# Kernel tuning notes

Hardware: AMD Instinct MI355X
Metric: run time of the kernel (lower is better)

The kernel has to match this reference:

```python
import jax, jax.numpy as jnp
import numpy as np

B, L, D, H = 2, 2048, 2048, 16
DH = D // H

def setup_inputs() -> dict:
    key = jax.random.key(0)
    ks = jax.random.split(key, 7)
    q = jax.random.normal(ks[0], (B, L, D), dtype=jnp.float32)
    k = jax.random.normal(ks[1], (B, L, D), dtype=jnp.float32)
    v = jax.random.normal(ks[2], (B, L, D), dtype=jnp.float32)
    # causal mask: True means masked (matches torch masked_fill semantics)
    attn_mask = jnp.triu(jnp.ones((L, L), dtype=bool), k=1)[None, None, :, :]
    scale = 0.02
    wq = jax.random.normal(ks[3], (D, D), dtype=jnp.float32) * scale
    wk = jax.random.normal(ks[4], (D, D), dtype=jnp.float32) * scale
    wv = jax.random.normal(ks[5], (D, D), dtype=jnp.float32) * scale
    wo = jax.random.normal(ks[6], (D, D), dtype=jnp.float32) * scale
    return {"q": q, "k": k, "v": v, "attn_mask": attn_mask,
            "wq": wq, "wk": wk, "wv": wv, "wo": wo}

def _split_heads(x):
    b, l, _ = x.shape
    return x.reshape(b, l, H, DH).transpose(0, 2, 1, 3)  # [B,H,L,DH]

def reference(q, k, v, attn_mask, wq, wk, wv, wo):
    # torch Linear: y = x @ W.T (bias=False)
    qh = _split_heads(q @ wq.T)
    kh = _split_heads(k @ wk.T)
    vh = _split_heads(v @ wv.T)
    scale = 1.0 / np.sqrt(DH).astype(np.float32)
    scores = jnp.einsum('bhqd,bhkd->bhqk', qh, kh) * scale
    neg = jnp.finfo(scores.dtype).min
    scores = jnp.where(attn_mask, neg, scores)
    attn = jax.nn.softmax(scores, axis=-1)
    ctx = jnp.einsum('bhqk,bhkd->bhqd', attn, vh)
    ctx = ctx.transpose(0, 2, 1, 3).reshape(q.shape[0], q.shape[1], D)
    return ctx @ wo.T
```

## Files before the change

### kernel.cpp

```cpp
#include <hip/hip_runtime.h>

#define B_  2
#define L_  2048
#define D_  2048
#define H_  16
#define DH_ 128
#define K_  2048

#define SCALEQ_ 0.12751734f

typedef __attribute__((ext_vector_type(8))) short bf16x8;
typedef __attribute__((ext_vector_type(4))) float f32x4;
typedef __attribute__((ext_vector_type(4))) float float4v;
typedef __attribute__((ext_vector_type(8))) unsigned short u16x8;
typedef __attribute__((ext_vector_type(4))) unsigned short u16x4;

__device__ __forceinline__ unsigned short f2bf(float f) {
  unsigned u = __builtin_bit_cast(unsigned, f);
  u += 0x7fffu + ((u >> 16) & 1u);
  return (unsigned short)(u >> 16);
}

__device__ __forceinline__ float exp2i(float x) {
  float r;
  asm("v_exp_f32 %0, %1" : "=v"(r) : "v"(x));
  return r;
}

typedef __attribute__((address_space(3))) unsigned int lds_uint;
typedef __attribute__((address_space(1))) const unsigned int glob_uint;
__device__ __forceinline__ void gld16(const void* g, void* l) {
  __builtin_amdgcn_global_load_lds((glob_uint*)g, (lds_uint*)l, 16, 0, 0);
}

#define BAR() do { asm volatile("" ::: "memory"); __builtin_amdgcn_s_barrier(); asm volatile("" ::: "memory"); } while (0)
#define VMCNT(n) asm volatile("s_waitcnt vmcnt(" #n ")" ::: "memory")

__global__ void cvt_all(const float* __restrict__ wq, const float* __restrict__ wk,
                        const float* __restrict__ wv, const float* __restrict__ wo,
                        const float* __restrict__ q, const float* __restrict__ k,
                        const float* __restrict__ v, unsigned short* __restrict__ ws,
                        int nacts) {
  const size_t DD = (size_t)D_ * D_;
  const size_t BLD = (size_t)B_ * L_ * D_;
  const int z = blockIdx.z;
  const float* src;
  unsigned short* dst;
  size_t nelem;
  if (z < 4) {
    src = (z == 0) ? wq : (z == 1) ? wk : (z == 2) ? wv : wo;
    dst = ws + (size_t)z * DD;
    nelem = DD;
  } else {
    if (z - 4 >= nacts) return;
    src = (z == 4) ? q : (z == 5) ? k : v;
    dst = ws + 4 * DD + (size_t)(z - 4) * BLD;
    nelem = BLD;
  }
  size_t i = ((size_t)blockIdx.x * 256 + threadIdx.x) * 8;
  if (i >= nelem) return;
  float4v x0 = *(const float4v*)(src + i);
  float4v x1 = *(const float4v*)(src + i + 4);
  u16x8 p;
  p[0]=f2bf(x0[0]); p[1]=f2bf(x0[1]); p[2]=f2bf(x0[2]); p[3]=f2bf(x0[3]);
  p[4]=f2bf(x1[0]); p[5]=f2bf(x1[1]); p[6]=f2bf(x1[2]); p[7]=f2bf(x1[3]);
  *(u16x8*)(dst + i) = p;
}

__global__ __launch_bounds__(512, 2) void gemm256(
    const unsigned short* __restrict__ a0, const unsigned short* __restrict__ a1,
    const unsigned short* __restrict__ w0, const unsigned short* __restrict__ w1,
    unsigned short* __restrict__ Kh, unsigned short* __restrict__ Vt) {
  __shared__ unsigned short smem[2 * 32768];

  const int lin = blockIdx.x + 16 * (blockIdx.y + 8 * blockIdx.z);
  const int s = (lin & 7) * 32 + (lin >> 3);
  const int mt = s & 15;
  const int r_ = s >> 4;
  const int ntile = r_ & 7;
  const int z = r_ >> 3;

  const unsigned short* A = z ? a1 : a0;
  const unsigned short* W = z ? w1 : w0;

  const int bm0 = mt * 256;
  const int bn0 = ntile * 256;

  const int tid = threadIdx.x;
  const int wid = tid >> 6, lane = tid & 63;
  const int wr = wid >> 2;
  const int wc = wid & 3;
  const int l15 = lane & 15, l4 = lane >> 4;

  const unsigned short* gsrc[8];
  int ldst[8];
#pragma unroll
  for (int i = 0; i < 4; ++i) {
    const int c = i * 512 + tid, r = c >> 3, s0 = c & 7;
    gsrc[i] = A + (size_t)(bm0 + r) * K_ + ((s0 ^ (r & 7)) << 3);
    ldst[i] = c * 8;
    gsrc[4 + i] = W + (size_t)(bn0 + r) * K_ + ((s0 ^ (r & 7)) << 3);
    ldst[4 + i] = 16384 + c * 8;
  }
#define STAGE(idx, p) do { gld16(gsrc[idx], &smem[(p) * 32768 + ldst[idx]]); gsrc[idx] += 64; } while (0)

  int offA[8][2], offB[4][2];
#pragma unroll
  for (int mf = 0; mf < 8; ++mf)
#pragma unroll
    for (int ks = 0; ks < 2; ++ks) {
      const int row = wr * 128 + mf * 16 + l15;
      const int ch = ks * 4 + l4;
      offA[mf][ks] = row * 64 + ((ch ^ (row & 7)) << 3);
    }
#pragma unroll
  for (int nf = 0; nf < 4; ++nf)
#pragma unroll
    for (int ks = 0; ks < 2; ++ks) {
      const int rowb = wc * 64 + nf * 16 + l15;
      const int ch = ks * 4 + l4;
      offB[nf][ks] = 16384 + rowb * 64 + ((ch ^ (rowb & 7)) << 3);
    }

  f32x4 acc[8][4];
#pragma unroll
  for (int m = 0; m < 8; ++m)
#pragma unroll
    for (int n = 0; n < 4; ++n) { f32x4 zz = {0.f, 0.f, 0.f, 0.f}; acc[m][n] = zz; }

  STAGE(0, 0); STAGE(1, 0); STAGE(2, 0); STAGE(3, 0);
  STAGE(4, 0); STAGE(5, 0); STAGE(6, 0); STAGE(7, 0);
  VMCNT(0);
  BAR();

  int p = 0;
  for (int t = 0; t < 32; ++t) {
    const int p2 = p ^ 1;
    if (t < 31) {
      STAGE(0, p2); STAGE(1, p2); STAGE(2, p2); STAGE(3, p2);
      STAGE(4, p2); STAGE(5, p2); STAGE(6, p2); STAGE(7, p2);
    }
    const unsigned short* bA = &smem[p * 32768];
    bf16x8 bfr[4][2];
#pragma unroll
    for (int nf = 0; nf < 4; ++nf)
#pragma unroll
      for (int ks = 0; ks < 2; ++ks)
        bfr[nf][ks] = *(const bf16x8*)&bA[offB[nf][ks]];
    __builtin_amdgcn_s_setprio(1);
#pragma unroll
    for (int mf = 0; mf < 8; ++mf) {
      bf16x8 a0f = *(const bf16x8*)&bA[offA[mf][0]];
      bf16x8 a1f = *(const bf16x8*)&bA[offA[mf][1]];
#pragma unroll
      for (int nf = 0; nf < 4; ++nf) {
        acc[mf][nf] = __builtin_amdgcn_mfma_f32_16x16x32_bf16(a0f, bfr[nf][0], acc[mf][nf], 0, 0, 0);
        acc[mf][nf] = __builtin_amdgcn_mfma_f32_16x16x32_bf16(a1f, bfr[nf][1], acc[mf][nf], 0, 0, 0);
      }
    }
    __builtin_amdgcn_s_setprio(0);
    VMCNT(0);
    BAR();
    p = p2;
  }
#undef STAGE

  if (z == 0) {
#pragma unroll
    for (int mf = 0; mf < 8; ++mf) {
      const int rr = bm0 + wr * 128 + mf * 16 + l4 * 4;
#pragma unroll
      for (int nf = 0; nf < 4; ++nf) {
        const int cc = bn0 + wc * 64 + nf * 16 + l15;
        const int h = cc >> 7, dh = cc & 127;
#pragma unroll
        for (int j = 0; j < 4; ++j) {
          const int r2 = rr + j;
          Kh[((size_t)((r2 >> 11) * H_ + h) * L_ + (r2 & 2047)) * DH_ + dh] = f2bf(acc[mf][nf][j]);
        }
      }
    }
  } else {
    unsigned short* T = smem;
    const int b = bm0 >> 11, lb = bm0 & 2047;
#pragma unroll 1
    for (int half = 0; half < 2; ++half) {
      if (half) __syncthreads();
      if (wr == half) {
#pragma unroll
        for (int mf = 0; mf < 8; ++mf) {
          const int rl = mf * 16 + l4 * 4;
#pragma unroll
          for (int nf = 0; nf < 4; ++nf) {
            const int cl = wc * 64 + nf * 16 + l15;
            u16x4 vv;
#pragma unroll
            for (int j = 0; j < 4; ++j) vv[j] = f2bf(acc[mf][nf][j]);
            *(u16x4*)&T[cl * 144 + rl] = vv;
          }
        }
      }
      __syncthreads();
#pragma unroll
      for (int it = 0; it < 8; ++it) {
        const int idx = it * 512 + tid;
        const int rT = idx >> 4, cT = idx & 15;
        u16x8 val = *(const u16x8*)&T[rT * 144 + cT * 8];
        const int n = bn0 + rT, h = n >> 7, dh = n & 127;
        *(u16x8*)&Vt[((size_t)(b * H_ + h) * DH_ + dh) * L_ + lb + half * 128 + cT * 8] = val;
      }
    }
  }
}

template <int OUT>
__global__ __launch_bounds__(512, 2) void gemm8p(
    const unsigned short* __restrict__ A, const unsigned short* __restrict__ W,
    void* __restrict__ outp) {
  __shared__ unsigned short smem[3 * 24576];

  const int lin = blockIdx.x + 32 * blockIdx.y;
  const int s = (lin & 7) * 32 + (lin >> 3);
  const int mt = s & 31;
  const int ntile = s >> 5;

  const int bm0 = mt * 128;
  const int bn0 = ntile * 256;

  const int tid = threadIdx.x;
  const int wid = tid >> 6, lane = tid & 63;
  const int wr = wid >> 2, wc = wid & 3;
  const int l15 = lane & 15, l4 = lane >> 4;

  const unsigned short* gsrc[6];
  int ldst[6];
  {
#pragma unroll
    for (int i = 0; i < 2; ++i) {
      const int c = i * 512 + tid, r = c >> 3, s0 = c & 7;
      gsrc[i] = A + (size_t)(bm0 + r) * K_ + ((s0 ^ (r & 7)) << 3);
      ldst[i] = c * 8;
    }
#pragma unroll
    for (int u = 0; u < 2; ++u)
#pragma unroll
      for (int i = 0; i < 2; ++i) {
        const int c = i * 512 + tid, r = c >> 3, s0 = c & 7;
        gsrc[2 + u * 2 + i] = W + (size_t)(bn0 + u * 128 + r) * K_ + ((s0 ^ (r & 7)) << 3);
        ldst[2 + u * 2 + i] = 8192 + (u * 1024 + c) * 8;
      }
  }
#define STAGE(idx, p) do { gld16(gsrc[idx], &smem[(p) * 24576 + ldst[idx]]); gsrc[idx] += 64; } while (0)

  int offA[4][2], offB[4][2];
#pragma unroll
  for (int mf = 0; mf < 4; ++mf)
#pragma unroll
    for (int ks = 0; ks < 2; ++ks) {
      const int row = wr * 64 + mf * 16 + l15;
      const int ch = ks * 4 + l4;
      offA[mf][ks] = row * 64 + ((ch ^ (row & 7)) << 3);
    }
#pragma unroll
  for (int nf = 0; nf < 4; ++nf)
#pragma unroll
    for (int ks = 0; ks < 2; ++ks) {
      const int rowb = wc * 64 + nf * 16 + l15;
      const int ch = ks * 4 + l4;
      offB[nf][ks] = 8192 + rowb * 64 + ((ch ^ (rowb & 7)) << 3);
    }

  f32x4 acc[4][4];
#pragma unroll
  for (int m = 0; m < 4; ++m)
#pragma unroll
    for (int n = 0; n < 4; ++n) { f32x4 zz = {0.f, 0.f, 0.f, 0.f}; acc[m][n] = zz; }

  STAGE(0, 0); STAGE(1, 0); STAGE(2, 0); STAGE(3, 0); STAGE(4, 0); STAGE(5, 0);
  STAGE(0, 1); STAGE(1, 1); STAGE(2, 1); STAGE(3, 1); STAGE(4, 1); STAGE(5, 1);
  VMCNT(6);
  BAR();

  int p = 0;
  for (int t = 0; t < 32; ++t) {
    int p2 = p + 2; if (p2 >= 3) p2 -= 3;
    const unsigned short* bA = &smem[p * 24576];
    bf16x8 af[4][2], bfr[4][2];
#pragma unroll
    for (int mf = 0; mf < 4; ++mf)
#pragma unroll
      for (int ks = 0; ks < 2; ++ks)
        af[mf][ks] = *(const bf16x8*)&bA[offA[mf][ks]];
#pragma unroll
    for (int nf = 0; nf < 4; ++nf)
#pragma unroll
      for (int ks = 0; ks < 2; ++ks)
        bfr[nf][ks] = *(const bf16x8*)&bA[offB[nf][ks]];
    if (t < 30) { STAGE(0, p2); STAGE(1, p2); STAGE(2, p2); STAGE(3, p2); STAGE(4, p2); STAGE(5, p2); }
    __builtin_amdgcn_s_setprio(1);
#pragma unroll
    for (int mf = 0; mf < 4; ++mf)
#pragma unroll
      for (int nf = 0; nf < 4; ++nf)
#pragma unroll
        for (int ks = 0; ks < 2; ++ks)
          acc[mf][nf] = __builtin_amdgcn_mfma_f32_16x16x32_bf16(af[mf][ks], bfr[nf][ks], acc[mf][nf], 0, 0, 0);
    __builtin_amdgcn_s_setprio(0);
    if (t < 30) { VMCNT(6); } else { VMCNT(0); }
    BAR();
    p = (p == 2) ? 0 : p + 1;
  }
#undef STAGE

  if (OUT == 0) {
    float* OF = (float*)outp;
#pragma unroll
    for (int mf = 0; mf < 4; ++mf) {
      const int rr = bm0 + wr * 64 + mf * 16 + l4 * 4;
#pragma unroll
      for (int nf = 0; nf < 4; ++nf) {
        const int cc = bn0 + wc * 64 + nf * 16 + l15;
#pragma unroll
        for (int j = 0; j < 4; ++j) OF[(size_t)(rr + j) * D_ + cc] = acc[mf][nf][j];
      }
    }
  } else {
    unsigned short* O = (unsigned short*)outp;
#pragma unroll
    for (int mf = 0; mf < 4; ++mf) {
      const int rr = bm0 + wr * 64 + mf * 16 + l4 * 4;
#pragma unroll
      for (int nf = 0; nf < 4; ++nf) {
        const int cc = bn0 + wc * 64 + nf * 16 + l15;
        const int h = cc >> 7, dh = cc & 127;
#pragma unroll
        for (int j = 0; j < 4; ++j) {
          const int r2 = rr + j;
          O[((size_t)((r2 >> 11) * H_ + h) * L_ + (r2 & 2047)) * DH_ + dh] = f2bf(acc[mf][nf][j] * SCALEQ_);
        }
      }
    }
  }
}

__global__ __launch_bounds__(256, 2) void proj_gemm_f32a(
    const float* __restrict__ q, const float* __restrict__ k, const float* __restrict__ v,
    const unsigned short* __restrict__ wqb, const unsigned short* __restrict__ wkb,
    const unsigned short* __restrict__ wvb,
    unsigned short* __restrict__ Qh, unsigned short* __restrict__ Kh,
    unsigned short* __restrict__ Vt) {
  __shared__ unsigned short smem[128 * 136];
  unsigned short* As = smem;
  unsigned short* Bs = smem + 128 * 64;

  const int z = blockIdx.z;
  const float* A = (z == 0) ? q : (z == 1) ? k : v;
  const unsigned short* W = (z == 0) ? wqb : (z == 1) ? wkb : wvb;

  const int tid = threadIdx.x;
  const int wave = tid >> 6, lane = tid & 63;
  const int wr = wave >> 1, wc = wave & 1;
  const int bm0 = blockIdx.x * 128;
  const int bn0 = blockIdx.y * 128;
  const int l15 = lane & 15, l4 = lane >> 4;

  f32x4 acc[4][4];
#pragma unroll
  for (int m = 0; m < 4; m++)
#pragma unroll
    for (int n = 0; n < 4; n++) { f32x4 zz = {0.f, 0.f, 0.f, 0.f}; acc[m][n] = zz; }

  for (int k0 = 0; k0 < K_; k0 += 64) {
#pragma unroll
    for (int it = 0; it < 4; ++it) {
      const int base = it * 256 + wave * 64;
      const int ch = base + lane;
      const int r = ch >> 3, c = ch & 7;
      gld16(W + (size_t)(bn0 + r) * K_ + (k0 + c * 8), Bs + base * 8);
    }
#pragma unroll
    for (int it = 0; it < 4; ++it) {
      const int ch = it * 256 + tid;
      const int r = ch >> 3, c = ch & 7;
      const float* g = A + (size_t)(bm0 + r) * K_ + (k0 + c * 8);
      float4v x0 = *(const float4v*)g;
      float4v x1 = *(const float4v*)(g + 4);
      u16x8 pp;
      pp[0]=f2bf(x0[0]); pp[1]=f2bf(x0[1]); pp[2]=f2bf(x0[2]); pp[3]=f2bf(x0[3]);
      pp[4]=f2bf(x1[0]); pp[5]=f2bf(x1[1]); pp[6]=f2bf(x1[2]); pp[7]=f2bf(x1[3]);
      *(u16x8*)&As[ch * 8] = pp;
    }
    __syncthreads();
#pragma unroll
    for (int ks = 0; ks < 2; ++ks) {
      const int kc = ks * 32 + l4 * 8;
      bf16x8 af[4], bfr[4];
#pragma unroll
      for (int m = 0; m < 4; m++) af[m] = *(const bf16x8*)&As[(wr * 64 + m * 16 + l15) * 64 + kc];
#pragma unroll
      for (int n = 0; n < 4; n++) bfr[n] = *(const bf16x8*)&Bs[(wc * 64 + n * 16 + l15) * 64 + kc];
#pragma unroll
      for (int m = 0; m < 4; m++)
#pragma unroll
        for (int n = 0; n < 4; n++)
          acc[m][n] = __builtin_amdgcn_mfma_f32_16x16x32_bf16(af[m], bfr[n], acc[m][n], 0, 0, 0);
    }
    __syncthreads();
  }

  if (z < 2) {
    unsigned short* O = (z == 0) ? Qh : Kh;
    const float qsc = (z == 0) ? SCALEQ_ : 1.f;
#pragma unroll
    for (int m = 0; m < 4; m++) {
      const int rr = bm0 + wr * 64 + m * 16 + l4 * 4;
#pragma unroll
      for (int n = 0; n < 4; n++) {
        const int cc = bn0 + wc * 64 + n * 16 + l15;
        const int h = cc >> 7, dh = cc & 127;
#pragma unroll
        for (int j = 0; j < 4; j++) {
          const int r2 = rr + j;
          O[((size_t)((r2 >> 11) * H_ + h) * L_ + (r2 & 2047)) * DH_ + dh] = f2bf(acc[m][n][j] * qsc);
        }
      }
    }
  } else {
    __syncthreads();
    unsigned short* T = smem;
#pragma unroll
    for (int m = 0; m < 4; m++)
#pragma unroll
      for (int n = 0; n < 4; n++) {
        const int cl = wc * 64 + n * 16 + l15;
        const int rl = wr * 64 + m * 16 + l4 * 4;
#pragma unroll
        for (int j = 0; j < 4; j++) T[cl * 136 + rl + j] = f2bf(acc[m][n][j]);
      }
    __syncthreads();
    const int b = bm0 >> 11, lbase = bm0 & 2047;
    const int hb = bn0 >> 7;
#pragma unroll
    for (int it = 0; it < 8; ++it) {
      const int idx = it * 256 + tid;
      const int dhl = idx >> 4, c = idx & 15;
      u16x8 val = *(const u16x8*)&T[dhl * 136 + c * 8];
      *(u16x8*)&Vt[((size_t)(b * H_ + hb) * DH_ + dhl) * L_ + lbase + c * 8] = val;
    }
  }
}

__global__ __launch_bounds__(512, 2) void attn_kernel(
    const unsigned short* __restrict__ Qh, const unsigned short* __restrict__ Kh,
    const unsigned short* __restrict__ Vt, unsigned short* __restrict__ ctx) {
  __shared__ unsigned short Ks[2][128 * 128];
  __shared__ unsigned short Vs[128 * 128];
  __shared__ unsigned short Ps[8][16 * 136];

  const int lin0 = blockIdx.x + 8 * blockIdx.y;
  const int w = (lin0 & 7) * 32 + (lin0 >> 3);
  const int pair = w & 7, bh = w >> 3;

  const size_t hoff = (size_t)bh * L_ * DH_;
  const unsigned short* Qp = Qh + hoff;
  const unsigned short* Kp = Kh + hoff;
  const unsigned short* Vp = Vt + hoff;

  const int tid = threadIdx.x, wave = tid >> 6, lane = tid & 63;
  const int l15 = lane & 15, l4 = lane >> 4;
  const int b = bh >> 4, h = bh & 15;

#define STAGEK(kt, buf) do { \
  _Pragma("unroll") \
  for (int it = 0; it < 4; ++it) { \
    const int ch = it * 512 + tid; \
    const int r = ch >> 4, s2 = ch & 15; \
    gld16(Kp + (size_t)((kt) * 128 + r) * DH_ + ((s2 ^ (r & 7)) * 8), (unsigned short*)&Ks[buf][0] + ch * 8); \
  } } while (0)
#define STAGEV(kt) do { \
  _Pragma("unroll") \
  for (int it = 0; it < 4; ++it) { \
    const int ch = it * 512 + tid; \
    const int r = ch >> 4, s2 = ch & 15; \
    gld16(Vp + (size_t)r * L_ + (kt) * 128 + ((s2 ^ (r & 7)) * 8), (unsigned short*)Vs + ch * 8); \
  } } while (0)

#pragma unroll 1
  for (int pp = 0; pp < 2; ++pp) {
    const int qt = pp ? (15 - pair) : pair;
    const int nt = qt + 1;

    bf16x8 qf[4];
    {
      const int qrow = qt * 128 + wave * 16 + l15;
#pragma unroll
      for (int s = 0; s < 4; s++)
        qf[s] = *(const bf16x8*)&Qp[(size_t)qrow * DH_ + s * 32 + l4 * 8];
    }

    f32x4 o[8];
#pragma unroll
    for (int df = 0; df < 8; df++) { f32x4 zz = {0.f, 0.f, 0.f, 0.f}; o[df] = zz; }
    float m_r = -1e30f;
    float l_r = 0.f;

    int p = 0;
    STAGEK(0, 0);
    VMCNT(0);
    BAR();

    const int qg = qt * 128 + wave * 16 + l15;
#pragma unroll 1
    for (int kt = 0; kt < nt; ++kt) {
      if (kt + 1 < nt) STAGEK(kt + 1, p ^ 1);
      STAGEV(kt);

      f32x4 sa[8];
#pragma unroll
      for (int f = 0; f < 8; f++) { f32x4 zz = {0.f, 0.f, 0.f, 0.f}; sa[f] = zz; }
      __builtin_amdgcn_s_setprio(1);
#pragma unroll
      for (int ks = 0; ks < 4; ++ks) {
        const int c = ks * 4 + l4;
#pragma unroll
        for (int f = 0; f < 8; ++f) {
          const int n = f * 16 + l15;
          bf16x8 kf = *(const bf16x8*)&Ks[p][n * 128 + ((c ^ (n & 7)) * 8)];
          sa[f] = __builtin_amdgcn_mfma_f32_16x16x32_bf16(kf, qf[ks], sa[f], 0, 0, 0);
        }
      }
      __builtin_amdgcn_s_setprio(0);

      if (kt == qt) {
#pragma unroll
        for (int f = 0; f < 8; f++) {
          const int kg = kt * 128 + f * 16 + l4 * 4;
#pragma unroll
          for (int j = 0; j < 4; j++)
            if (kg + j > qg) sa[f][j] = -1e30f;
        }
      }

      float mx = -1e30f;
#pragma unroll
      for (int f = 0; f < 8; f++)
#pragma unroll
        for (int j = 0; j < 4; j++) mx = fmaxf(mx, sa[f][j]);
      mx = fmaxf(mx, __shfl_xor(mx, 16));
      mx = fmaxf(mx, __shfl_xor(mx, 32));

      if (!__all(mx <= m_r + 8.f)) {
        const float mnew = fmaxf(m_r, mx);
        const float alpha = exp2i(m_r - mnew);
        l_r *= alpha;
        m_r = mnew;
#pragma unroll
        for (int j = 0; j < 4; j++) {
          const float aj = __shfl(alpha, l4 * 4 + j);
#pragma unroll
          for (int df = 0; df < 8; df++) o[df][j] *= aj;
        }
      }

      float rs = 0.f;
#pragma unroll
      for (int f = 0; f < 8; f++) {
        u16x4 pk4;
#pragma unroll
        for (int j = 0; j < 4; j++) {
          float pv = exp2i(sa[f][j] - m_r);
          rs += pv;
          pk4[j] = f2bf(pv);
        }
        *(u16x4*)&Ps[wave][l15 * 136 + f * 16 + l4 * 4] = pk4;
      }
      rs += __shfl_xor(rs, 16);
      rs += __shfl_xor(rs, 32);
      l_r += rs;

      VMCNT(0);
      BAR();

      __builtin_amdgcn_s_setprio(1);
#pragma unroll
      for (int ksl = 0; ksl < 4; ++ksl) {
        const int pc = ksl * 4 + l4;
        bf16x8 pf = *(const bf16x8*)&Ps[wave][l15 * 136 + ksl * 32 + l4 * 8];
#pragma unroll
        for (int df = 0; df < 8; ++df) {
          const int vr = df * 16 + l15;
          bf16x8 vf = *(const bf16x8*)&Vs[vr * 128 + ((pc ^ (vr & 7)) * 8)];
          o[df] = __builtin_amdgcn_mfma_f32_16x16x32_bf16(pf, vf, o[df], 0, 0, 0);
        }
      }
      __builtin_amdgcn_s_setprio(0);
      BAR();
      p ^= 1;
    }

#pragma unroll
    for (int j = 0; j < 4; j++) {
      const float inv = 1.0f / __shfl(l_r, l4 * 4 + j);
      const int lq = qt * 128 + wave * 16 + l4 * 4 + j;
      const size_t rowb = ((size_t)(b * L_ + lq)) * D_ + h * DH_;
#pragma unroll
      for (int df = 0; df < 8; ++df)
        ctx[rowb + df * 16 + l15] = f2bf(o[df][j] * inv);
    }
  }
#undef STAGEK
#undef STAGEV
}

extern "C" void kernel_launch(void* const* d_in, const int* in_sizes, int n_in,
                              void* d_out, int out_size, void* d_ws, size_t ws_size,
                              hipStream_t stream) {
  const float* q  = (const float*)d_in[0];
  const float* k  = (const float*)d_in[1];
  const float* v  = (const float*)d_in[2];
  const float* wq = (const float*)d_in[4];
  const float* wk = (const float*)d_in[5];
  const float* wv = (const float*)d_in[6];
  const float* wo = (const float*)d_in[7];

  const size_t DD = (size_t)D_ * D_;
  const size_t BLD = (size_t)B_ * L_ * D_;
  unsigned short* ws  = (unsigned short*)d_ws;
  unsigned short* wqb = ws;
  unsigned short* wkb = wqb + DD;
  unsigned short* wvb = wkb + DD;
  unsigned short* wob = wvb + DD;

  const size_t need_full = (4 * DD + 7 * BLD) * 2;

  if (ws_size >= need_full) {
    unsigned short* qb  = wob + DD;
    unsigned short* kb  = qb + BLD;
    unsigned short* vb  = kb + BLD;
    unsigned short* QhP = vb + BLD;
    unsigned short* KhP = QhP + BLD;
    unsigned short* VtP = KhP + BLD;
    unsigned short* ctx = VtP + BLD;

    cvt_all<<<dim3(4096, 1, 7), 256, 0, stream>>>(wq, wk, wv, wo, q, k, v, ws, 3);
    gemm256<<<dim3(16, 8, 2), 512, 0, stream>>>(kb, vb, wkb, wvb, KhP, VtP);
    gemm8p<1><<<dim3(32, 8), 512, 0, stream>>>(qb, wqb, QhP);
    attn_kernel<<<dim3(8, 32), 512, 0, stream>>>(QhP, KhP, VtP, ctx);
    gemm8p<0><<<dim3(32, 8), 512, 0, stream>>>(ctx, wob, d_out);
  } else {
    unsigned short* QhP = wob + DD;
    unsigned short* KhP = QhP + BLD;
    unsigned short* VtP = KhP + BLD;
    unsigned short* ctx = VtP + BLD;

    cvt_all<<<dim3(4096, 1, 4), 256, 0, stream>>>(wq, wk, wv, wo, q, k, v, ws, 0);
    proj_gemm_f32a<<<dim3(32, 16, 3), 256, 0, stream>>>(q, k, v, wqb, wkb, wvb, QhP, KhP, VtP);
    attn_kernel<<<dim3(8, 32), 512, 0, stream>>>(QhP, KhP, VtP, ctx);
    gemm8p<0><<<dim3(32, 8), 512, 0, stream>>>(ctx, wob, d_out);
  }
}
```

Before: 246.3 us.

## Switch K/V projection GEMM to triple-buffered K=32 stages with prefetch depth two

The K/V projection GEMM moves from two LDS buffers of K=64 to three buffers of K=32. Loads run two stages ahead, and the wait becomes vmcnt(4) instead of a full drain. This is meant to hide global-load latency behind MFMA work without growing LDS. In exchange it doubles the number of iterations and barriers, and the smaller K chunks need a new 4-way XOR swizzle that may change LDS bank-conflict behaviour.

Result: no change. 249.5 us (+1.3%).

```diff
diff --git a/kernel.cpp b/kernel.cpp
--- a/kernel.cpp
+++ b/kernel.cpp
@@ -71,7 +71,7 @@
     const unsigned short* __restrict__ a0, const unsigned short* __restrict__ a1,
     const unsigned short* __restrict__ w0, const unsigned short* __restrict__ w1,
     unsigned short* __restrict__ Kh, unsigned short* __restrict__ Vt) {
-  __shared__ unsigned short smem[2 * 32768];
+  __shared__ unsigned short smem[3 * 16384];
 
   const int lin = blockIdx.x + 16 * (blockIdx.y + 8 * blockIdx.z);
   const int s = (lin & 7) * 32 + (lin >> 3);
@@ -92,35 +92,29 @@
   const int wc = wid & 3;
   const int l15 = lane & 15, l4 = lane >> 4;
 
-  const unsigned short* gsrc[8];
-  int ldst[8];
-#pragma unroll
-  for (int i = 0; i < 4; ++i) {
-    const int c = i * 512 + tid, r = c >> 3, s0 = c & 7;
-    gsrc[i] = A + (size_t)(bm0 + r) * K_ + ((s0 ^ (r & 7)) << 3);
+  const unsigned short* gsrc[4];
+  int ldst[4];
+#pragma unroll
+  for (int i = 0; i < 2; ++i) {
+    const int c = i * 512 + tid, r = c >> 2, s0 = c & 3;
+    gsrc[i] = A + (size_t)(bm0 + r) * K_ + ((s0 ^ (r & 3)) << 3);
     ldst[i] = c * 8;
-    gsrc[4 + i] = W + (size_t)(bn0 + r) * K_ + ((s0 ^ (r & 7)) << 3);
-    ldst[4 + i] = 16384 + c * 8;
-  }
-#define STAGE(idx, p) do { gld16(gsrc[idx], &smem[(p) * 32768 + ldst[idx]]); gsrc[idx] += 64; } while (0)
-
-  int offA[8][2], offB[4][2];
-#pragma unroll
-  for (int mf = 0; mf < 8; ++mf)
-#pragma unroll
-    for (int ks = 0; ks < 2; ++ks) {
-      const int row = wr * 128 + mf * 16 + l15;
-      const int ch = ks * 4 + l4;
-      offA[mf][ks] = row * 64 + ((ch ^ (row & 7)) << 3);
-    }
-#pragma unroll
-  for (int nf = 0; nf < 4; ++nf)
-#pragma unroll
-    for (int ks = 0; ks < 2; ++ks) {
-      const int rowb = wc * 64 + nf * 16 + l15;
-      const int ch = ks * 4 + l4;
-      offB[nf][ks] = 16384 + rowb * 64 + ((ch ^ (rowb & 7)) << 3);
-    }
+    gsrc[2 + i] = W + (size_t)(bn0 + r) * K_ + ((s0 ^ (r & 3)) << 3);
+    ldst[2 + i] = 8192 + c * 8;
+  }
+#define STAGE(idx, p) do { gld16(gsrc[idx], &smem[(p) * 16384 + ldst[idx]]); gsrc[idx] += 32; } while (0)
+
+  int offA[8], offB[4];
+#pragma unroll
+  for (int mf = 0; mf < 8; ++mf) {
+    const int row = wr * 128 + mf * 16 + l15;
+    offA[mf] = row * 32 + ((l4 ^ (row & 3)) << 3);
+  }
+#pragma unroll
+  for (int nf = 0; nf < 4; ++nf) {
+    const int rowb = wc * 64 + nf * 16 + l15;
+    offB[nf] = 8192 + rowb * 32 + ((l4 ^ (rowb & 3)) << 3);
+  }
 
   f32x4 acc[8][4];
 #pragma unroll
@@ -129,39 +123,30 @@
     for (int n = 0; n < 4; ++n) { f32x4 zz = {0.f, 0.f, 0.f, 0.f}; acc[m][n] = zz; }
 
   STAGE(0, 0); STAGE(1, 0); STAGE(2, 0); STAGE(3, 0);
-  STAGE(4, 0); STAGE(5, 0); STAGE(6, 0); STAGE(7, 0);
-  VMCNT(0);
+  STAGE(0, 1); STAGE(1, 1); STAGE(2, 1); STAGE(3, 1);
+  VMCNT(4);
   BAR();
 
   int p = 0;
-  for (int t = 0; t < 32; ++t) {
-    const int p2 = p ^ 1;
-    if (t < 31) {
-      STAGE(0, p2); STAGE(1, p2); STAGE(2, p2); STAGE(3, p2);
-      STAGE(4, p2); STAGE(5, p2); STAGE(6, p2); STAGE(7, p2);
-    }
-    const unsigned short* bA = &smem[p * 32768];
-    bf16x8 bfr[4][2];
-#pragma unroll
-    for (int nf = 0; nf < 4; ++nf)
-#pragma unroll
-      for (int ks = 0; ks < 2; ++ks)
-        bfr[nf][ks] = *(const bf16x8*)&bA[offB[nf][ks]];
+  for (int t = 0; t < 64; ++t) {
+    int p2 = p + 2; if (p2 >= 3) p2 -= 3;
+    const unsigned short* bA = &smem[p * 16384];
+    bf16x8 bfr[4];
+#pragma unroll
+    for (int nf = 0; nf < 4; ++nf) bfr[nf] = *(const bf16x8*)&bA[offB[nf]];
+    if (t < 62) { STAGE(0, p2); STAGE(1, p2); STAGE(2, p2); STAGE(3, p2); }
     __builtin_amdgcn_s_setprio(1);
 #pragma unroll
     for (int mf = 0; mf < 8; ++mf) {
-      bf16x8 a0f = *(const bf16x8*)&bA[offA[mf][0]];
-      bf16x8 a1f = *(const bf16x8*)&bA[offA[mf][1]];
-#pragma unroll
-      for (int nf = 0; nf < 4; ++nf) {
-        acc[mf][nf] = __builtin_amdgcn_mfma_f32_16x16x32_bf16(a0f, bfr[nf][0], acc[mf][nf], 0, 0, 0);
-        acc[mf][nf] = __builtin_amdgcn_mfma_f32_16x16x32_bf16(a1f, bfr[nf][1], acc[mf][nf], 0, 0, 0);
-      }
+      bf16x8 af = *(const bf16x8*)&bA[offA[mf]];
+#pragma unroll
+      for (int nf = 0; nf < 4; ++nf)
+        acc[mf][nf] = __builtin_amdgcn_mfma_f32_16x16x32_bf16(af, bfr[nf], acc[mf][nf], 0, 0, 0);
     }
     __builtin_amdgcn_s_setprio(0);
-    VMCNT(0);
+    if (t < 62) { VMCNT(4); } else { VMCNT(0); }
     BAR();
-    p = p2;
+    p = (p == 2) ? 0 : p + 1;
   }
 #undef STAGE
 
```
